# Kernel optimization log

Measured on AMD Instinct MI355X. Metric: run time of the kernel, lower is better.

The kernel has to match this reference:

```python
import jax, jax.numpy as jnp
import numpy as np

N_NODES = 100000


def gcn_conv(x, W, b, src, dst, num_nodes):
    # PyG GCNConv: add self-loops, symmetric normalization, x @ W, scatter-add, + b
    xw = x @ W  # [N, out]
    loop = jnp.arange(num_nodes, dtype=src.dtype)
    s = jnp.concatenate([src, loop])  # message source j
    d = jnp.concatenate([dst, loop])  # aggregation target i
    deg = jax.ops.segment_sum(jnp.ones_like(d, dtype=xw.dtype), d, num_segments=num_nodes)
    dis = jnp.where(deg > 0, jax.lax.rsqrt(deg), 0.0)  # D^{-1/2}
    norm = dis[s] * dis[d]  # [E+N]
    msg = norm[:, None] * xw[s]  # gather + scale
    out = jax.ops.segment_sum(msg, d, num_segments=num_nodes)  # scatter-add
    return out + b


def setup_inputs() -> dict:
    key = jax.random.key(0)
    k1, k2, k3, k4 = jax.random.split(key, 4)
    F, H, E = 64, 64, 1250000
    x = jax.random.normal(k1, (N_NODES, F), dtype=jnp.float32)
    edge_index = jax.random.randint(k2, (2, E), 0, N_NODES, dtype=jnp.int64)
    W1 = jax.random.normal(k3, (F, H), dtype=jnp.float32) * (1.0 / np.sqrt(F))
    b1 = jnp.zeros((H,), dtype=jnp.float32)
    W2 = jax.random.normal(k4, (H, F), dtype=jnp.float32) * (1.0 / np.sqrt(H))
    b2 = jnp.zeros((F,), dtype=jnp.float32)
    return {"x": x, "edge_index": edge_index, "W1": W1, "b1": b1, "W2": W2, "b2": b2}


def reference(x, edge_index, W1, b1, W2, b2):
    src, dst = edge_index[0], edge_index[1]
    h = gcn_conv(x, W1, b1, src, dst, N_NODES)
    h = jax.nn.relu(h)
    out = gcn_conv(h, W2, b2, src, dst, N_NODES)
    return out
```

## Files before the change

kernel.cpp:

```cpp
#include <hip/hip_runtime.h>

#define NN    100000
#define F     64
#define NBUCK 391
#define CAPB  4096
#define TILE  4096

#define O_CURSOR 0
#define O_ROWPTR 512
#define O_DEG    100864
#define O_DIS    201216
#define O_PACKED 301568
#define O_SRT    1903104
#define O_AH     3504768
#define O_HH     6704768

__device__ __forceinline__ unsigned bf_rne(float x) {
    unsigned u = __float_as_uint(x);
    return (u + 0x7FFFu + ((u >> 16) & 1u)) >> 16;
}
__device__ __forceinline__ unsigned pack2(float lo, float hi) {
    return bf_rne(lo) | (bf_rne(hi) << 16);
}
__device__ __forceinline__ float lo_f(unsigned u) { return __uint_as_float(u << 16); }
__device__ __forceinline__ float hi_f(unsigned u) { return __uint_as_float(u & 0xFFFF0000u); }

struct BpSmem {
    int hist[NBUCK], lofs[NBUCK], gbase[NBUCK], lcur[NBUCK];
    int wsum[8];
    unsigned stage[TILE];
    unsigned short sbuck[TILE];
};
union KSmem {
    BpSmem bp;
    float wl[64 * 64];
};

__device__ __forceinline__ void binpack_body(const int* __restrict__ src,
                                             const int* __restrict__ dst, int E,
                                             int* __restrict__ cursor,
                                             unsigned* __restrict__ packed,
                                             int bid, BpSmem& sm) {
    int t  = threadIdx.x;
    int t0 = bid * TILE;
    int n  = min(TILE, E - t0);

    if (t < NBUCK) sm.hist[t] = 0;
    __syncthreads();
    for (int i = t; i < n; i += 512) atomicAdd(&sm.hist[dst[t0 + i] >> 8], 1);
    __syncthreads();
    int lane = t & 63, w = t >> 6;
    int v = (t < NBUCK) ? sm.hist[t] : 0;
    int s = v;
#pragma unroll
    for (int off = 1; off < 64; off <<= 1) {
        int u = __shfl_up(s, off, 64);
        if (lane >= off) s += u;
    }
    if (lane == 63) sm.wsum[w] = s;
    __syncthreads();
    if (t == 0) {
        int run = 0;
#pragma unroll
        for (int i = 0; i < 8; ++i) { int c = sm.wsum[i]; sm.wsum[i] = run; run += c; }
    }
    __syncthreads();
    if (t < NBUCK) {
        int ex = s - v + sm.wsum[w];
        sm.lofs[t] = ex;
        sm.lcur[t] = ex;
        sm.gbase[t] = t * CAPB + (v ? atomicAdd(&cursor[t], v) : 0);
    }
    __syncthreads();
    for (int i = t; i < n; i += 512) {
        int d = dst[t0 + i];
        int b = d >> 8;
        int p = atomicAdd(&sm.lcur[b], 1);
        sm.stage[p] = ((unsigned)src[t0 + i] << 8) | (unsigned)(d & 255);
        sm.sbuck[p] = (unsigned short)b;
    }
    __syncthreads();
    for (int i = t; i < n; i += 512) {
        int b = sm.sbuck[i];
        packed[sm.gbase[b] + (i - sm.lofs[b])] = sm.stage[i];
    }
}

__device__ __forceinline__ void gemm_body(const float* __restrict__ X,
                                          const float* __restrict__ W,
                                          unsigned* __restrict__ Ah, int bid,
                                          float* wl) {
    int t = threadIdx.x;
    for (int i = t; i < 64 * 64; i += 512) wl[i] = W[i];
    __syncthreads();
    int lane = t & 63;
    int w    = t >> 6;
    float Wreg[64];
#pragma unroll
    for (int k = 0; k < 64; ++k) Wreg[k] = wl[k * 64 + lane];

    int row0 = bid * 32 + w * 4;
    const float* xp = X + (size_t)row0 * F;
    float xa = xp[lane];
    float xb = xp[64 + lane];
    float xc = xp[128 + lane];
    float xd = xp[192 + lane];
    float a0 = 0.f, a1 = 0.f, a2 = 0.f, a3 = 0.f;
#pragma unroll
    for (int k = 0; k < 64; ++k) {
        float wv = Wreg[k];
        a0 = fmaf(__uint_as_float(__builtin_amdgcn_readlane(__float_as_uint(xa), k)), wv, a0);
        a1 = fmaf(__uint_as_float(__builtin_amdgcn_readlane(__float_as_uint(xb), k)), wv, a1);
        a2 = fmaf(__uint_as_float(__builtin_amdgcn_readlane(__float_as_uint(xc), k)), wv, a2);
        a3 = fmaf(__uint_as_float(__builtin_amdgcn_readlane(__float_as_uint(xd), k)), wv, a3);
    }
    float p0 = __shfl_xor(a0, 1, 64);
    float p1 = __shfl_xor(a1, 1, 64);
    float p2 = __shfl_xor(a2, 1, 64);
    float p3 = __shfl_xor(a3, 1, 64);
    if (!(lane & 1)) {
        int c = lane >> 1;
        Ah[(size_t)(row0 + 0) * 32 + c] = pack2(a0, p0);
        Ah[(size_t)(row0 + 1) * 32 + c] = pack2(a1, p1);
        Ah[(size_t)(row0 + 2) * 32 + c] = pack2(a2, p2);
        Ah[(size_t)(row0 + 3) * 32 + c] = pack2(a3, p3);
    }
}

__device__ __forceinline__ void gemm_h_body(const unsigned* __restrict__ Hh,
                                            const float* __restrict__ W,
                                            unsigned* __restrict__ Ah, int bid,
                                            float* wl) {
    int t = threadIdx.x;
    for (int i = t; i < 64 * 64; i += 512) wl[i] = W[i];
    __syncthreads();
    int lane = t & 63;
    int w    = t >> 6;
    float Wreg[64];
#pragma unroll
    for (int k = 0; k < 64; ++k) Wreg[k] = wl[k * 64 + lane];

    int row0 = bid * 32 + w * 4;
    int l = lane & 31, r = lane >> 5;
    unsigned pa = Hh[(size_t)(row0 + r) * 32 + l];
    unsigned pb = Hh[(size_t)(row0 + 2 + r) * 32 + l];
    float a0 = 0.f, a1 = 0.f, a2 = 0.f, a3 = 0.f;
#pragma unroll
    for (int k = 0; k < 64; ++k) {
        float wv = Wreg[k];
        unsigned q0 = __builtin_amdgcn_readlane(pa, k >> 1);
        unsigned q1 = __builtin_amdgcn_readlane(pa, 32 + (k >> 1));
        unsigned q2 = __builtin_amdgcn_readlane(pb, k >> 1);
        unsigned q3 = __builtin_amdgcn_readlane(pb, 32 + (k >> 1));
        float x0 = (k & 1) ? hi_f(q0) : lo_f(q0);
        float x1 = (k & 1) ? hi_f(q1) : lo_f(q1);
        float x2 = (k & 1) ? hi_f(q2) : lo_f(q2);
        float x3 = (k & 1) ? hi_f(q3) : lo_f(q3);
        a0 = fmaf(x0, wv, a0);
        a1 = fmaf(x1, wv, a1);
        a2 = fmaf(x2, wv, a2);
        a3 = fmaf(x3, wv, a3);
    }
    float p0 = __shfl_xor(a0, 1, 64);
    float p1 = __shfl_xor(a1, 1, 64);
    float p2 = __shfl_xor(a2, 1, 64);
    float p3 = __shfl_xor(a3, 1, 64);
    if (!(lane & 1)) {
        int c = lane >> 1;
        Ah[(size_t)(row0 + 0) * 32 + c] = pack2(a0, p0);
        Ah[(size_t)(row0 + 1) * 32 + c] = pack2(a1, p1);
        Ah[(size_t)(row0 + 2) * 32 + c] = pack2(a2, p2);
        Ah[(size_t)(row0 + 3) * 32 + c] = pack2(a3, p3);
    }
}

__global__ __launch_bounds__(512) void pre_gemm1(const int* __restrict__ src,
                                                 const int* __restrict__ dst, int E,
                                                 int nbp, int* __restrict__ cursor,
                                                 unsigned* __restrict__ packed,
                                                 const float* __restrict__ X,
                                                 const float* __restrict__ W1,
                                                 unsigned* __restrict__ Ah) {
    __shared__ KSmem sm;
    if ((int)blockIdx.x < nbp)
        binpack_body(src, dst, E, cursor, packed, blockIdx.x, sm.bp);
    else
        gemm_body(X, W1, Ah, blockIdx.x - nbp, sm.wl);
}

__global__ __launch_bounds__(512) void gemm2h(const unsigned* __restrict__ Hh,
                                              const float* __restrict__ W,
                                              unsigned* __restrict__ Ah) {
    __shared__ float wl[64 * 64];
    gemm_h_body(Hh, W, Ah, blockIdx.x, wl);
}

__global__ __launch_bounds__(512) void node_sort(const unsigned* __restrict__ packed,
                                                 const int* __restrict__ cursor,
                                                 int* __restrict__ row_ptr,
                                                 int* __restrict__ deg,
                                                 float* __restrict__ dis,
                                                 int* __restrict__ srt) {
    __shared__ int h[256];
    __shared__ int lcur[256];
    __shared__ int wsum[4];
    __shared__ int stage[CAPB];
    int b = blockIdx.x, t = threadIdx.x;
    int nbase = b << 8;
    int nloc = min(256, NN - nbase);
    int beg = b * CAPB;
    int n = cursor[b];

    if (t < 256) h[t] = 0;
    __syncthreads();
    for (int i = t; i < n; i += 512)
        atomicAdd(&h[packed[beg + i] & 255u], 1);
    __syncthreads();
    int lane = t & 63, w = t >> 6;
    int v = 0, s = 0;
    if (t < 256) { v = h[t]; s = v; }
#pragma unroll
    for (int off = 1; off < 64; off <<= 1) {
        int u = __shfl_up(s, off, 64);
        if (lane >= off) s += u;
    }
    if (t < 256 && lane == 63) wsum[w] = s;
    __syncthreads();
    if (t == 0) {
        int run = 0;
#pragma unroll
        for (int i = 0; i < 4; ++i) { int c = wsum[i]; wsum[i] = run; run += c; }
    }
    __syncthreads();
    if (t < 256) {
        int e0 = s - v + wsum[w];
        lcur[t] = e0;
        if (t < nloc) {
            row_ptr[nbase + t] = beg + e0;
            deg[nbase + t]     = v;
            dis[nbase + t]     = rsqrtf((float)v + 1.0f);
        }
    }
    __syncthreads();
    for (int i = t; i < n; i += 512) {
        unsigned p = packed[beg + i];
        int pos = atomicAdd(&lcur[p & 255u], 1);
        stage[pos] = (int)(p >> 8);
    }
    __syncthreads();
    for (int i = t; i < n; i += 512) srt[beg + i] = stage[i];
}

template <int MODE>
__global__ __launch_bounds__(256) void agg_out(const uint2* __restrict__ Ah2,
                                               const int* __restrict__ row_ptr,
                                               const int* __restrict__ deg,
                                               const int* __restrict__ srt,
                                               const float* __restrict__ dis,
                                               const float* __restrict__ bias,
                                               void* __restrict__ outp) {
    int sub  = threadIdx.x & 15;
    int node = blockIdx.x * 16 + (threadIdx.x >> 4);
    int beg = row_ptr[node];
    int end = beg + deg[node];
    float di = dis[node];
    uint2 su = Ah2[(size_t)node * 16 + sub];
    float4 acc;
    acc.x = di * lo_f(su.x);
    acc.y = di * hi_f(su.x);
    acc.z = di * lo_f(su.y);
    acc.w = di * hi_f(su.y);
    int j = beg;
    for (; j + 4 <= end; j += 4) {
        int s0 = srt[j], s1 = srt[j + 1], s2 = srt[j + 2], s3 = srt[j + 3];
        float d0 = dis[s0], d1 = dis[s1], d2 = dis[s2], d3 = dis[s3];
        uint2 g0 = Ah2[(size_t)s0 * 16 + sub];
        uint2 g1 = Ah2[(size_t)s1 * 16 + sub];
        uint2 g2 = Ah2[(size_t)s2 * 16 + sub];
        uint2 g3 = Ah2[(size_t)s3 * 16 + sub];
        acc.x = fmaf(d0, lo_f(g0.x), fmaf(d1, lo_f(g1.x), fmaf(d2, lo_f(g2.x), fmaf(d3, lo_f(g3.x), acc.x))));
        acc.y = fmaf(d0, hi_f(g0.x), fmaf(d1, hi_f(g1.x), fmaf(d2, hi_f(g2.x), fmaf(d3, hi_f(g3.x), acc.y))));
        acc.z = fmaf(d0, lo_f(g0.y), fmaf(d1, lo_f(g1.y), fmaf(d2, lo_f(g2.y), fmaf(d3, lo_f(g3.y), acc.z))));
        acc.w = fmaf(d0, hi_f(g0.y), fmaf(d1, hi_f(g1.y), fmaf(d2, hi_f(g2.y), fmaf(d3, hi_f(g3.y), acc.w))));
    }
    for (; j < end; ++j) {
        int s0 = srt[j];
        float d0 = dis[s0];
        uint2 g0 = Ah2[(size_t)s0 * 16 + sub];
        acc.x = fmaf(d0, lo_f(g0.x), acc.x);
        acc.y = fmaf(d0, hi_f(g0.x), acc.y);
        acc.z = fmaf(d0, lo_f(g0.y), acc.z);
        acc.w = fmaf(d0, hi_f(g0.y), acc.w);
    }
    float4 bb = ((const float4*)bias)[sub];
    float4 o;
    o.x = fmaf(di, acc.x, bb.x);
    o.y = fmaf(di, acc.y, bb.y);
    o.z = fmaf(di, acc.z, bb.z);
    o.w = fmaf(di, acc.w, bb.w);
    if (MODE == 1) {
        o.x = fmaxf(o.x, 0.f); o.y = fmaxf(o.y, 0.f);
        o.z = fmaxf(o.z, 0.f); o.w = fmaxf(o.w, 0.f);
        uint2 pk;
        pk.x = pack2(o.x, o.y);
        pk.y = pack2(o.z, o.w);
        ((uint2*)outp)[(size_t)node * 16 + sub] = pk;
    } else {
        ((float4*)outp)[(size_t)node * 16 + sub] = o;
    }
}

extern "C" void kernel_launch(void* const* d_in, const int* in_sizes, int n_in,
                              void* d_out, int out_size, void* d_ws, size_t ws_size,
                              hipStream_t stream) {
    const float* x  = (const float*)d_in[0];
    const int*   ei = (const int*)d_in[1];
    const float* W1 = (const float*)d_in[2];
    const float* b1 = (const float*)d_in[3];
    const float* W2 = (const float*)d_in[4];
    const float* b2 = (const float*)d_in[5];
    float* out = (float*)d_out;
    int E = in_sizes[1] / 2;
    const int* src = ei;
    const int* dst = ei + E;

    int*      ws_i    = (int*)d_ws;
    int*      cursor  = ws_i + O_CURSOR;
    int*      row_ptr = ws_i + O_ROWPTR;
    int*      deg     = ws_i + O_DEG;
    float*    dis     = (float*)(ws_i + O_DIS);
    unsigned* packed  = (unsigned*)(ws_i + O_PACKED);
    int*      srt     = ws_i + O_SRT;
    unsigned* Ah      = (unsigned*)(ws_i + O_AH);
    unsigned* Hh      = (unsigned*)(ws_i + O_HH);

    int nbp = (E + TILE - 1) / TILE;

    hipMemsetAsync(cursor, 0, NBUCK * sizeof(int), stream);
    pre_gemm1<<<nbp + NN / 32, 512, 0, stream>>>(src, dst, E, nbp, cursor, packed,
                                                 x, W1, Ah);
    node_sort<<<NBUCK, 512, 0, stream>>>(packed, cursor, row_ptr, deg, dis, srt);
    agg_out<1><<<NN / 16, 256, 0, stream>>>((const uint2*)Ah, row_ptr, deg, srt,
                                            dis, b1, Hh);
    gemm2h<<<NN / 32, 512, 0, stream>>>(Hh, W2, Ah);
    agg_out<0><<<NN / 16, 256, 0, stream>>>((const uint2*)Ah, row_ptr, deg, srt,
                                            dis, b2, out);
}
```

Baseline: 213.3 us.

## Fuse all GCN stages into one persistent cooperative kernel with grid syncs

Replaces the memset plus five separate kernel launches with a single cooperative persistent kernel of 1024 blocks. The blocks loop over the binpack/GEMM1, node sort, aggregation, GEMM2 and final aggregation stages, separated by grid-wide barriers. Aggregation now uses 512-thread blocks covering 32 nodes each. The aim is to remove per-launch overhead and the tail bubbles between kernels. The cost is grid-sync overhead, a fixed grid that may be poorly balanced (only 391 blocks do work in node sort), and register pressure from the 8-waves launch bound; a non-cooperative fallback path is kept.

```diff
diff --git a/kernel.cpp b/kernel.cpp
--- a/kernel.cpp
+++ b/kernel.cpp
@@ -1,10 +1,15 @@
 #include <hip/hip_runtime.h>
+#include <hip/hip_cooperative_groups.h>
+namespace cg = cooperative_groups;
 
 #define NN    100000
 #define F     64
 #define NBUCK 391
 #define CAPB  4096
 #define TILE  4096
+#define GRID  1024
+#define BS    512
+#define NGU   (NN / 32)
 
 #define O_CURSOR 0
 #define O_ROWPTR 512
@@ -31,9 +36,14 @@
     unsigned stage[TILE];
     unsigned short sbuck[TILE];
 };
+struct NsSmem {
+    int h[256], lcur[256], wsum[4];
+    int stage[CAPB];
+};
 union KSmem {
     BpSmem bp;
-    float wl[64 * 64];
+    NsSmem ns;
+    float  wl[64 * 64];
 };
 
 __device__ __forceinline__ void binpack_body(const int* __restrict__ src,
@@ -47,7 +57,7 @@
 
     if (t < NBUCK) sm.hist[t] = 0;
     __syncthreads();
-    for (int i = t; i < n; i += 512) atomicAdd(&sm.hist[dst[t0 + i] >> 8], 1);
+    for (int i = t; i < n; i += BS) atomicAdd(&sm.hist[dst[t0 + i] >> 8], 1);
     __syncthreads();
     int lane = t & 63, w = t >> 6;
     int v = (t < NBUCK) ? sm.hist[t] : 0;
@@ -72,7 +82,7 @@
         sm.gbase[t] = t * CAPB + (v ? atomicAdd(&cursor[t], v) : 0);
     }
     __syncthreads();
-    for (int i = t; i < n; i += 512) {
+    for (int i = t; i < n; i += BS) {
         int d = dst[t0 + i];
         int b = d >> 8;
         int p = atomicAdd(&sm.lcur[b], 1);
@@ -80,7 +90,7 @@
         sm.sbuck[p] = (unsigned short)b;
     }
     __syncthreads();
-    for (int i = t; i < n; i += 512) {
+    for (int i = t; i < n; i += BS) {
         int b = sm.sbuck[i];
         packed[sm.gbase[b] + (i - sm.lofs[b])] = sm.stage[i];
     }
@@ -91,7 +101,7 @@
                                           unsigned* __restrict__ Ah, int bid,
                                           float* wl) {
     int t = threadIdx.x;
-    for (int i = t; i < 64 * 64; i += 512) wl[i] = W[i];
+    for (int i = t; i < 64 * 64; i += BS) wl[i] = W[i];
     __syncthreads();
     int lane = t & 63;
     int w    = t >> 6;
@@ -132,7 +142,7 @@
                                             unsigned* __restrict__ Ah, int bid,
                                             float* wl) {
     int t = threadIdx.x;
-    for (int i = t; i < 64 * 64; i += 512) wl[i] = W[i];
+    for (int i = t; i < 64 * 64; i += BS) wl[i] = W[i];
     __syncthreads();
     int lane = t & 63;
     int w    = t >> 6;
@@ -174,67 +184,43 @@
     }
 }
 
-__global__ __launch_bounds__(512) void pre_gemm1(const int* __restrict__ src,
-                                                 const int* __restrict__ dst, int E,
-                                                 int nbp, int* __restrict__ cursor,
-                                                 unsigned* __restrict__ packed,
-                                                 const float* __restrict__ X,
-                                                 const float* __restrict__ W1,
-                                                 unsigned* __restrict__ Ah) {
-    __shared__ KSmem sm;
-    if ((int)blockIdx.x < nbp)
-        binpack_body(src, dst, E, cursor, packed, blockIdx.x, sm.bp);
-    else
-        gemm_body(X, W1, Ah, blockIdx.x - nbp, sm.wl);
-}
-
-__global__ __launch_bounds__(512) void gemm2h(const unsigned* __restrict__ Hh,
-                                              const float* __restrict__ W,
-                                              unsigned* __restrict__ Ah) {
-    __shared__ float wl[64 * 64];
-    gemm_h_body(Hh, W, Ah, blockIdx.x, wl);
-}
-
-__global__ __launch_bounds__(512) void node_sort(const unsigned* __restrict__ packed,
-                                                 const int* __restrict__ cursor,
-                                                 int* __restrict__ row_ptr,
-                                                 int* __restrict__ deg,
-                                                 float* __restrict__ dis,
-                                                 int* __restrict__ srt) {
-    __shared__ int h[256];
-    __shared__ int lcur[256];
-    __shared__ int wsum[4];
-    __shared__ int stage[CAPB];
-    int b = blockIdx.x, t = threadIdx.x;
+__device__ __forceinline__ void node_sort_body(const unsigned* __restrict__ packed,
+                                               const int* __restrict__ cursor,
+                                               int* __restrict__ row_ptr,
+                                               int* __restrict__ deg,
+                                               float* __restrict__ dis,
+                                               int* __restrict__ srt,
+                                               int b, NsSmem& sm) {
+    int t = threadIdx.x;
     int nbase = b << 8;
     int nloc = min(256, NN - nbase);
     int beg = b * CAPB;
     int n = cursor[b];
 
-    if (t < 256) h[t] = 0;
-    __syncthreads();
-    for (int i = t; i < n; i += 512)
-        atomicAdd(&h[packed[beg + i] & 255u], 1);
+    if (t < 256) sm.h[t] = 0;
+    __syncthreads();
+    for (int i = t; i < n; i += BS)
+        atomicAdd(&sm.h[packed[beg + i] & 255u], 1);
     __syncthreads();
     int lane = t & 63, w = t >> 6;
     int v = 0, s = 0;
-    if (t < 256) { v = h[t]; s = v; }
+    if (t < 256) { v = sm.h[t]; s = v; }
 #pragma unroll
     for (int off = 1; off < 64; off <<= 1) {
         int u = __shfl_up(s, off, 64);
         if (lane >= off) s += u;
     }
-    if (t < 256 && lane == 63) wsum[w] = s;
+    if (t < 256 && lane == 63) sm.wsum[w] = s;
     __syncthreads();
     if (t == 0) {
         int run = 0;
 #pragma unroll
-        for (int i = 0; i < 4; ++i) { int c = wsum[i]; wsum[i] = run; run += c; }
+        for (int i = 0; i < 4; ++i) { int c = sm.wsum[i]; sm.wsum[i] = run; run += c; }
     }
     __syncthreads();
     if (t < 256) {
-        int e0 = s - v + wsum[w];
-        lcur[t] = e0;
+        int e0 = s - v + sm.wsum[w];
+        sm.lcur[t] = e0;
         if (t < nloc) {
             row_ptr[nbase + t] = beg + e0;
             deg[nbase + t]     = v;
@@ -242,25 +228,25 @@
         }
     }
     __syncthreads();
-    for (int i = t; i < n; i += 512) {
+    for (int i = t; i < n; i += BS) {
         unsigned p = packed[beg + i];
-        int pos = atomicAdd(&lcur[p & 255u], 1);
-        stage[pos] = (int)(p >> 8);
-    }
-    __syncthreads();
-    for (int i = t; i < n; i += 512) srt[beg + i] = stage[i];
+        int pos = atomicAdd(&sm.lcur[p & 255u], 1);
+        sm.stage[pos] = (int)(p >> 8);
+    }
+    __syncthreads();
+    for (int i = t; i < n; i += BS) srt[beg + i] = sm.stage[i];
 }
 
 template <int MODE>
-__global__ __launch_bounds__(256) void agg_out(const uint2* __restrict__ Ah2,
-                                               const int* __restrict__ row_ptr,
-                                               const int* __restrict__ deg,
-                                               const int* __restrict__ srt,
-                                               const float* __restrict__ dis,
-                                               const float* __restrict__ bias,
-                                               void* __restrict__ outp) {
+__device__ __forceinline__ void agg_body(const uint2* __restrict__ Ah2,
+                                         const int* __restrict__ row_ptr,
+                                         const int* __restrict__ deg,
+                                         const int* __restrict__ srt,
+                                         const float* __restrict__ dis,
+                                         const float* __restrict__ bias,
+                                         void* __restrict__ outp, int g) {
     int sub  = threadIdx.x & 15;
-    int node = blockIdx.x * 16 + (threadIdx.x >> 4);
+    int node = g * 32 + (threadIdx.x >> 4);
     int beg = row_ptr[node];
     int end = beg + deg[node];
     float di = dis[node];
@@ -310,6 +296,73 @@
     }
 }
 
+__global__ __launch_bounds__(BS, 8) void gcn_fused(
+        const int* src, const int* dst, int E, int nbp,
+        int* cursor, unsigned* packed, int* row_ptr, int* deg, float* dis,
+        int* srt, unsigned* Ah, unsigned* Hh,
+        const float* x, const float* W1, const float* b1,
+        const float* W2, const float* b2, float* out) {
+    cg::grid_group gg = cg::this_grid();
+    __shared__ KSmem sm;
+    int bid = blockIdx.x;
+    int t   = threadIdx.x;
+
+    if (bid == 0 && t < NBUCK) cursor[t] = 0;
+    gg.sync();
+
+    for (int wk = bid; wk < nbp + NGU; wk += GRID) {
+        if (wk < nbp) binpack_body(src, dst, E, cursor, packed, wk, sm.bp);
+        else          gemm_body(x, W1, Ah, wk - nbp, sm.wl);
+        __syncthreads();
+    }
+    gg.sync();
+
+    if (bid < NBUCK) node_sort_body(packed, cursor, row_ptr, deg, dis, srt, bid, sm.ns);
+    gg.sync();
+
+    for (int g = bid; g < NGU; g += GRID)
+        agg_body<1>((const uint2*)Ah, row_ptr, deg, srt, dis, b1, Hh, g);
+    gg.sync();
+
+    for (int g = bid; g < NGU; g += GRID) {
+        gemm_h_body(Hh, W2, Ah, g, sm.wl);
+        __syncthreads();
+    }
+    gg.sync();
+
+    for (int g = bid; g < NGU; g += GRID)
+        agg_body<0>((const uint2*)Ah, row_ptr, deg, srt, dis, b2, out, g);
+}
+
+__global__ __launch_bounds__(BS) void fb_pre_gemm1(const int* src, const int* dst,
+                                                   int E, int nbp, int* cursor,
+                                                   unsigned* packed, const float* x,
+                                                   const float* W1, unsigned* Ah) {
+    __shared__ KSmem sm;
+    if ((int)blockIdx.x < nbp)
+        binpack_body(src, dst, E, cursor, packed, blockIdx.x, sm.bp);
+    else
+        gemm_body(x, W1, Ah, blockIdx.x - nbp, sm.wl);
+}
+__global__ __launch_bounds__(BS) void fb_node_sort(const unsigned* packed,
+                                                   const int* cursor, int* row_ptr,
+                                                   int* deg, float* dis, int* srt) {
+    __shared__ NsSmem sm;
+    node_sort_body(packed, cursor, row_ptr, deg, dis, srt, blockIdx.x, sm);
+}
+template <int MODE>
+__global__ __launch_bounds__(BS) void fb_agg(const uint2* Ah2, const int* row_ptr,
+                                             const int* deg, const int* srt,
+                                             const float* dis, const float* bias,
+                                             void* outp) {
+    agg_body<MODE>(Ah2, row_ptr, deg, srt, dis, bias, outp, blockIdx.x);
+}
+__global__ __launch_bounds__(BS) void fb_gemm2h(const unsigned* Hh, const float* W,
+                                                unsigned* Ah) {
+    __shared__ float wl[64 * 64];
+    gemm_h_body(Hh, W, Ah, blockIdx.x, wl);
+}
+
 extern "C" void kernel_launch(void* const* d_in, const int* in_sizes, int n_in,
                               void* d_out, int out_size, void* d_ws, size_t ws_size,
                               hipStream_t stream) {
@@ -336,13 +389,23 @@
 
     int nbp = (E + TILE - 1) / TILE;
 
-    hipMemsetAsync(cursor, 0, NBUCK * sizeof(int), stream);
-    pre_gemm1<<<nbp + NN / 32, 512, 0, stream>>>(src, dst, E, nbp, cursor, packed,
-                                                 x, W1, Ah);
-    node_sort<<<NBUCK, 512, 0, stream>>>(packed, cursor, row_ptr, deg, dis, srt);
-    agg_out<1><<<NN / 16, 256, 0, stream>>>((const uint2*)Ah, row_ptr, deg, srt,
-                                            dis, b1, Hh);
-    gemm2h<<<NN / 32, 512, 0, stream>>>(Hh, W2, Ah);
-    agg_out<0><<<NN / 16, 256, 0, stream>>>((const uint2*)Ah, row_ptr, deg, srt,
-                                            dis, b2, out);
-}
+    void* kargs[] = {
+        (void*)&src, (void*)&dst, (void*)&E, (void*)&nbp,
+        (void*)&cursor, (void*)&packed, (void*)&row_ptr, (void*)&deg,
+        (void*)&dis, (void*)&srt, (void*)&Ah, (void*)&Hh,
+        (void*)&x, (void*)&W1, (void*)&b1, (void*)&W2, (void*)&b2, (void*)&out
+    };
+    hipError_t err = hipLaunchCooperativeKernel((void*)gcn_fused, dim3(GRID),
+                                                dim3(BS), kargs, 0, stream);
+    if (err != hipSuccess) {
+        hipMemsetAsync(cursor, 0, NBUCK * sizeof(int), stream);
+        fb_pre_gemm1<<<nbp + NGU, BS, 0, stream>>>(src, dst, E, nbp, cursor, packed,
+                                                   x, W1, Ah);
+        fb_node_sort<<<NBUCK, BS, 0, stream>>>(packed, cursor, row_ptr, deg, dis, srt);
+        fb_agg<1><<<NGU, BS, 0, stream>>>((const uint2*)Ah, row_ptr, deg, srt, dis,
+                                          b1, Hh);
+        fb_gemm2h<<<NGU, BS, 0, stream>>>(Hh, W2, Ah);
+        fb_agg<0><<<NGU, BS, 0, stream>>>((const uint2*)Ah, row_ptr, deg, srt, dis,
+                                          b2, out);
+    }
+}
```

Result: slower. 804.4 us (+277.0%).
